# Kernel tuning notes

Measured on AMD Instinct MI355X. Metric: run time of the kernel, lower is better.

The kernel has to match this reference:

```python
import jax, jax.numpy as jnp
import numpy as np

B, F, N, NO = 1, 512, 8192, 21
L1, L2, L3 = 640, 256, 128


def setup_inputs() -> dict:
    key = jax.random.key(0)
    ks = jax.random.split(key, 32)
    rn = lambda k, s: jax.random.normal(k, s, dtype=jnp.float32)
    inp = {
        "emb1": rn(ks[0], (B, F, N)),
        "emb2": rn(ks[1], (B, F, N)),
        "t1": rn(ks[2], (B, 3, N)),
        "t2": rn(ks[3], (B, 3, N)),
        "obj": jax.random.randint(ks[4], (B, 1), 0, NO, dtype=jnp.int32),
    }
    # 1x1 Conv1d weights == dense (out,in) matrices + bias
    dims_r = [(L1, 2 * F), (L2, L1), (L3, L2), (NO * 4, L3)]
    dims_t = [(L1, 2 * F), (L2, L1), (L3, L2), (NO * 3, L3)]
    ki = 5
    for br, dims in (("r", dims_r), ("t", dims_t)):
        for i, (o, c) in enumerate(dims, start=1):
            inp[f"w{i}{br}"] = rn(ks[ki], (o, c)) * (1.0 / np.sqrt(c)); ki += 1
            inp[f"b{i}{br}"] = rn(ks[ki], (o,)) * 0.01; ki += 1
    return inp


def _knn1(ref, qry):
    # ref, qry: (3, N). For each query point j, index of nearest ref point.
    g = ref.T @ qry  # (N_ref, N_qry)
    d2 = jnp.sum(ref * ref, axis=0)[:, None] + jnp.sum(qry * qry, axis=0)[None, :] - 2.0 * g
    return jnp.argmin(d2, axis=0)  # (N_qry,)


def _branch(x, w1, b1, w2, b2, w3, b3, w4, b4):
    h = jax.nn.relu(w1 @ x + b1[:, None])
    h = jax.nn.relu(w2 @ h + b2[:, None])
    h = jax.nn.relu(w3 @ h + b3[:, None])
    return w4 @ h + b4[:, None]


def reference(emb1, emb2, t1, t2, obj,
              w1r, b1r, w2r, b2r, w3r, b3r, w4r, b4r,
              w1t, b1t, w2t, b2t, w3t, b3t, w4t, b4t):
    bs, num_feat, num_points = emb1.shape
    t1 = t1.reshape(bs, 3, -1)
    t2 = t2.reshape(bs, 3, -1)
    # brute-force 1-NN of each t2 point among t1 points (bs == 1)
    idx = _knn1(t1[0], t2[0])  # (N,) zero-based (torch code subtracts 1 from 1-based inds)
    emb1g = emb1[0][:, idx]  # gather matched features, (F, N)
    # torch.stack([emb1,emb2],dim=1).view(bs, 2F, N) == channel concat [emb1g; emb2]
    emb = jnp.concatenate([emb1g, emb2[0]], axis=0)  # (2F, N)
    rx = _branch(emb, w1r, b1r, w2r, b2r, w3r, b3r, w4r, b4r).reshape(NO, 4, num_points)
    tx = _branch(emb, w1t, b1t, w2t, b2t, w3t, b3t, w4t, b4t).reshape(NO, 3, num_points)
    obj0 = obj[0]  # (1,)
    out_rx = jnp.transpose(rx[obj0], (0, 2, 1))  # (1, N, 4)
    out_tx = jnp.transpose(tx[obj0], (0, 2, 1))  # (1, N, 3)
    return out_rx, out_tx
```

## Files before the change

kernel.cpp:

```cpp
#include <hip/hip_runtime.h>

typedef unsigned short u16;
typedef __bf16 bf16x8 __attribute__((ext_vector_type(8)));
typedef float f32x4 __attribute__((ext_vector_type(4)));

__device__ __forceinline__ float b2f(u16 v) {
    return __uint_as_float(((unsigned int)v) << 16);
}
__device__ __forceinline__ u16 f2b(float f) {
    unsigned int u = __float_as_uint(f);
    u += 0x7fffu + ((u >> 16) & 1u);
    return (u16)(u >> 16);
}

__device__ __forceinline__ void ld_lds16(const u16* g, u16* l) {
    __builtin_amdgcn_global_load_lds(
        (__attribute__((address_space(1))) void*)(uintptr_t)(const void*)g,
        (__attribute__((address_space(3))) void*)l, 16, 0, 0);
}

__global__ void pack_w_k(const float* __restrict__ w1r, const float* __restrict__ w1t,
                         const float* __restrict__ w2r, const float* __restrict__ w2t,
                         const float* __restrict__ w3r, const float* __restrict__ w3t,
                         u16* __restrict__ dst)
{
    size_t i = (size_t)blockIdx.x * 2048 + (size_t)threadIdx.x * 8;
    const float* src; size_t off;
    if (i < 655360)       { src = w1r; off = 0; }
    else if (i < 1310720) { src = w1t; off = 655360; }
    else if (i < 1474560) { src = w2r; off = 1310720; }
    else if (i < 1638400) { src = w2t; off = 1474560; }
    else if (i < 1671168) { src = w3r; off = 1638400; }
    else                  { src = w3t; off = 1671168; }
    const float4 lo = *(const float4*)(src + (i - off));
    const float4 hi = *(const float4*)(src + (i - off) + 4);
    ushort4 o0, o1;
    o0.x = f2b(lo.x); o0.y = f2b(lo.y); o0.z = f2b(lo.z); o0.w = f2b(lo.w);
    o1.x = f2b(hi.x); o1.y = f2b(hi.y); o1.z = f2b(hi.z); o1.w = f2b(hi.w);
    *(ushort4*)(dst + i) = o0;
    *(ushort4*)(dst + i + 4) = o1;
}

__global__ void knn_k(const float* __restrict__ t1, const float* __restrict__ t2,
                      unsigned long long* __restrict__ keys)
{
    __shared__ float4 ref[128];
    const int t = threadIdx.x;
    const int rs = blockIdx.x;
    const int qb = blockIdx.y;
    if (t < 128) {
        int i = rs * 128 + t;
        float x = t1[i], y = t1[8192 + i], z = t1[16384 + i];
        float rr = __fadd_rn(__fadd_rn(__fmul_rn(x, x), __fmul_rn(y, y)), __fmul_rn(z, z));
        ref[t] = make_float4(x, y, z, rr);
    }
    __syncthreads();

    float qx[8], qy[8], qz[8], qq[8], bestd[8];
    int besti[8];
    const int q0 = qb * 2048 + t;
#pragma unroll
    for (int j = 0; j < 8; ++j) {
        int q = q0 + j * 256;
        qx[j] = t2[q]; qy[j] = t2[8192 + q]; qz[j] = t2[16384 + q];
        qq[j] = __fadd_rn(__fadd_rn(__fmul_rn(qx[j], qx[j]), __fmul_rn(qy[j], qy[j])),
                          __fmul_rn(qz[j], qz[j]));
        bestd[j] = __uint_as_float(0x7f800000u);
        besti[j] = 0;
    }
    for (int i = 0; i < 128; ++i) {
        float4 r = ref[i];
        int ridx = rs * 128 + i;
#pragma unroll
        for (int j = 0; j < 8; ++j) {
            float g = __fmaf_rn(qz[j], r.z, __fmaf_rn(qy[j], r.y, __fmul_rn(qx[j], r.x)));
            float d2 = __fsub_rn(__fadd_rn(r.w, qq[j]), __fmul_rn(2.0f, g));
            if (d2 < bestd[j]) { bestd[j] = d2; besti[j] = ridx; }
        }
    }
#pragma unroll
    for (int j = 0; j < 8; ++j) {
        unsigned long long key =
            ((unsigned long long)__float_as_uint(bestd[j]) << 32) | (unsigned int)besti[j];
        atomicMin(&keys[q0 + j * 256], key);
    }
}

__global__ void transpose_k(const float* __restrict__ e1, const float* __restrict__ e2,
                            u16* __restrict__ o1, u16* __restrict__ o2)
{
    __shared__ float tile[64][65];
    const float* in = blockIdx.z ? e2 : e1;
    u16* out = blockIdx.z ? o2 : o1;
    const int ostride = blockIdx.z ? 1024 : 512;
    const int coff = blockIdx.z ? 512 : 0;
    const int t = threadIdx.x;
    const int n0 = blockIdx.x * 64, f0 = blockIdx.y * 64;
    const int c = t & 63, r4 = t >> 6;
#pragma unroll
    for (int p = 0; p < 16; ++p) {
        int fr = p * 4 + r4;
        tile[fr][c] = in[(size_t)(f0 + fr) * 8192 + n0 + c];
    }
    __syncthreads();
    const int fc = (t & 15) * 4;
    const int nr4 = t >> 4;
#pragma unroll
    for (int p = 0; p < 4; ++p) {
        int nr = p * 16 + nr4;
        ushort4 o;
        o.x = f2b(tile[fc + 0][nr]); o.y = f2b(tile[fc + 1][nr]);
        o.z = f2b(tile[fc + 2][nr]); o.w = f2b(tile[fc + 3][nr]);
        *(ushort4*)&out[(size_t)(n0 + nr) * ostride + coff + f0 + fc] = o;
    }
}

__global__ void gather_k(const unsigned long long* __restrict__ keys,
                         const u16* __restrict__ emb1t, u16* __restrict__ Xt)
{
    const int t = threadIdx.x, w = t >> 6, l = t & 63;
    const int nbase = blockIdx.x * 32;
#pragma unroll
    for (int it = 0; it < 8; ++it) {
        int n = nbase + it * 4 + w;
        int i = (int)(keys[n] & 0xffffffffu);
        const uint4* src = (const uint4*)(emb1t + (size_t)i * 512);
        uint4* dst = (uint4*)(Xt + (size_t)n * 1024);
        dst[l] = src[l];
    }
}

template <int TN>
__global__ __launch_bounds__(256) void gemm_bt(
    const u16* __restrict__ Ar, const u16* __restrict__ At,
    const float* __restrict__ biasr, const float* __restrict__ biast,
    const u16* __restrict__ Bt, u16* __restrict__ Ct,
    int Mh, int K, int bstride, int b_step, int ostride, int relu)
{
    constexpr int NJ = TN / 32;
    __shared__ __align__(16) u16 lds_a[128 * 32];
    __shared__ __align__(16) u16 lds_b[TN * 32];

    const int t = threadIdx.x;
    const int n0 = blockIdx.x * TN;
    const int m0 = blockIdx.y * 128;
    const int branch = blockIdx.z;

    const u16* A = branch ? At : Ar;
    const float* bias = branch ? biast : biasr;
    const int b_off = branch * b_step;
    const int out_off = branch * Mh;

    const int w = t >> 6, l = t & 63;
    const int sr = l >> 2, sc = (l & 3) * 8;

    const u16* gA0 = A + (size_t)(m0 + w * 32 + sr) * K + sc;
    const u16* gA1 = gA0 + (size_t)16 * K;
    u16* lA0 = &lds_a[w * 1024];
    u16* lA1 = lA0 + 512;

    const u16* gB0;
    const u16* gB1 = nullptr;
    u16 *lB0, *lB1 = nullptr;
    if (TN == 128) {
        gB0 = Bt + (size_t)(n0 + w * 32 + sr) * bstride + b_off + sc;
        gB1 = gB0 + (size_t)16 * bstride;
        lB0 = &lds_b[w * 1024];
        lB1 = lB0 + 512;
    } else {
        gB0 = Bt + (size_t)(n0 + w * 16 + sr) * bstride + b_off + sc;
        lB0 = &lds_b[w * 512];
    }

    const int wm = (w & 1) * 64;
    const int wn = (w >> 1) * (TN / 2);
    const int lrow = l & 15, quad = l >> 4;
    const u16* fa = &lds_a[(wm + lrow) * 32 + quad * 8];
    const u16* fb = &lds_b[(wn + lrow) * 32 + quad * 8];

    f32x4 acc[4][NJ];
#pragma unroll
    for (int i = 0; i < 4; ++i)
#pragma unroll
        for (int j = 0; j < NJ; ++j)
            acc[i][j] = (f32x4){0.f, 0.f, 0.f, 0.f};

    ld_lds16(gA0, lA0); ld_lds16(gA1, lA1);
    ld_lds16(gB0, lB0);
    if (TN == 128) ld_lds16(gB1, lB1);

    for (int kt = 0; kt < K; kt += 32) {
        __syncthreads();
        bf16x8 af[4], bfr[NJ];
#pragma unroll
        for (int i = 0; i < 4; ++i) af[i] = *(const bf16x8*)(fa + i * 16 * 32);
#pragma unroll
        for (int j = 0; j < NJ; ++j) bfr[j] = *(const bf16x8*)(fb + j * 16 * 32);
        __syncthreads();
        if (kt + 32 < K) {
            gA0 += 32; gA1 += 32; gB0 += 32;
            ld_lds16(gA0, lA0); ld_lds16(gA1, lA1);
            ld_lds16(gB0, lB0);
            if (TN == 128) { gB1 += 32; ld_lds16(gB1, lB1); }
        }
#pragma unroll
        for (int i = 0; i < 4; ++i)
#pragma unroll
            for (int j = 0; j < NJ; ++j)
                acc[i][j] = __builtin_amdgcn_mfma_f32_16x16x32_bf16(
                    af[i], bfr[j], acc[i][j], 0, 0, 0);
    }

#pragma unroll
    for (int i = 0; i < 4; ++i) {
        const int mbase = m0 + wm + i * 16 + quad * 4;
        const float4 bbv = *(const float4*)&bias[mbase];
#pragma unroll
        for (int j = 0; j < NJ; ++j) {
            const int n = n0 + wn + j * 16 + lrow;
            f32x4 v = acc[i][j];
            float x0 = v[0] + bbv.x, x1 = v[1] + bbv.y;
            float x2 = v[2] + bbv.z, x3 = v[3] + bbv.w;
            if (relu) {
                x0 = fmaxf(x0, 0.f); x1 = fmaxf(x1, 0.f);
                x2 = fmaxf(x2, 0.f); x3 = fmaxf(x3, 0.f);
            }
            ushort4 o;
            o.x = f2b(x0); o.y = f2b(x1); o.z = f2b(x2); o.w = f2b(x3);
            *(ushort4*)&Ct[(size_t)n * ostride + out_off + mbase] = o;
        }
    }
}

__global__ __launch_bounds__(256) void gemm3_final_k(
    const u16* __restrict__ Ar, const u16* __restrict__ At,
    const float* __restrict__ b3r, const float* __restrict__ b3t,
    const u16* __restrict__ Bt,
    const float* __restrict__ w4r, const float* __restrict__ b4r,
    const float* __restrict__ w4t, const float* __restrict__ b4t,
    const int* __restrict__ objp, float* __restrict__ out)
{
    __shared__ __align__(16) u16 lds_a[128 * 32];
    __shared__ __align__(16) u16 lds_b[64 * 32];
    __shared__ __align__(16) float lds_h[64 * 132];
    __shared__ __align__(16) float lds_w[4 * 132];

    const int t = threadIdx.x;
    const int n0 = blockIdx.x * 64;
    const int branch = blockIdx.y;

    const u16* A = branch ? At : Ar;
    const float* bias = branch ? b3t : b3r;
    const int b_off = branch * 256;

    const int w = t >> 6, l = t & 63;
    const int sr = l >> 2, sc = (l & 3) * 8;

    const u16* gA0 = A + (size_t)(w * 32 + sr) * 256 + sc;
    const u16* gA1 = gA0 + (size_t)16 * 256;
    u16* lA0 = &lds_a[w * 1024];
    u16* lA1 = lA0 + 512;

    const u16* gB0 = Bt + (size_t)(n0 + w * 16 + sr) * 512 + b_off + sc;
    u16* lB0 = &lds_b[w * 512];

    const int wm = (w & 1) * 64;
    const int wn = (w >> 1) * 32;
    const int lrow = l & 15, quad = l >> 4;
    const u16* fa = &lds_a[(wm + lrow) * 32 + quad * 8];
    const u16* fb = &lds_b[(wn + lrow) * 32 + quad * 8];

    f32x4 acc[4][2];
#pragma unroll
    for (int i = 0; i < 4; ++i)
#pragma unroll
        for (int j = 0; j < 2; ++j)
            acc[i][j] = (f32x4){0.f, 0.f, 0.f, 0.f};

    ld_lds16(gA0, lA0); ld_lds16(gA1, lA1);
    ld_lds16(gB0, lB0);

    for (int kt = 0; kt < 256; kt += 32) {
        __syncthreads();
        bf16x8 af[4], bfr[2];
#pragma unroll
        for (int i = 0; i < 4; ++i) af[i] = *(const bf16x8*)(fa + i * 16 * 32);
#pragma unroll
        for (int j = 0; j < 2; ++j) bfr[j] = *(const bf16x8*)(fb + j * 16 * 32);
        __syncthreads();
        if (kt + 32 < 256) {
            gA0 += 32; gA1 += 32; gB0 += 32;
            ld_lds16(gA0, lA0); ld_lds16(gA1, lA1);
            ld_lds16(gB0, lB0);
        }
#pragma unroll
        for (int i = 0; i < 4; ++i)
#pragma unroll
            for (int j = 0; j < 2; ++j)
                acc[i][j] = __builtin_amdgcn_mfma_f32_16x16x32_bf16(
                    af[i], bfr[j], acc[i][j], 0, 0, 0);
    }

#pragma unroll
    for (int i = 0; i < 4; ++i) {
        const int mbase = wm + i * 16 + quad * 4;
        const float4 bbv = *(const float4*)&bias[mbase];
#pragma unroll
        for (int j = 0; j < 2; ++j) {
            const int nl = wn + j * 16 + lrow;
            f32x4 v = acc[i][j];
            float4 x;
            x.x = fmaxf(v[0] + bbv.x, 0.f); x.y = fmaxf(v[1] + bbv.y, 0.f);
            x.z = fmaxf(v[2] + bbv.z, 0.f); x.w = fmaxf(v[3] + bbv.w, 0.f);
            *(float4*)&lds_h[nl * 132 + mbase] = x;
        }
    }
    const int o = objp[0];
    const int NR = branch ? 3 : 4;
    const float* w4 = branch ? w4t : w4r;
    if (t < 128) {
        for (int r = 0; r < NR; ++r)
            lds_w[r * 132 + t] = w4[(size_t)(o * NR + r) * 128 + t];
    }
    __syncthreads();

    const int nl = t >> 2, k = t & 3;
    if (k < NR) {
        const float4* hp = (const float4*)&lds_h[nl * 132];
        const float4* wp4 = (const float4*)&lds_w[k * 132];
        float s = 0.f;
#pragma unroll
        for (int m4 = 0; m4 < 32; ++m4) {
            float4 h = hp[m4], ww = wp4[m4];
            s = fmaf(h.x, ww.x, s); s = fmaf(h.y, ww.y, s);
            s = fmaf(h.z, ww.z, s); s = fmaf(h.w, ww.w, s);
        }
        const int n = n0 + nl;
        if (branch == 0) out[(size_t)n * 4 + k] = s + b4r[o * 4 + k];
        else             out[32768 + (size_t)n * 3 + k] = s + b4t[o * 3 + k];
    }
}

extern "C" void kernel_launch(void* const* d_in, const int* in_sizes, int n_in,
                              void* d_out, int out_size, void* d_ws, size_t ws_size,
                              hipStream_t stream)
{
    const float* emb1 = (const float*)d_in[0];
    const float* emb2 = (const float*)d_in[1];
    const float* t1   = (const float*)d_in[2];
    const float* t2   = (const float*)d_in[3];
    const int*   obj  = (const int*)d_in[4];
    const float* w1r = (const float*)d_in[5];  const float* b1r = (const float*)d_in[6];
    const float* w2r = (const float*)d_in[7];  const float* b2r = (const float*)d_in[8];
    const float* w3r = (const float*)d_in[9];  const float* b3r = (const float*)d_in[10];
    const float* w4r = (const float*)d_in[11]; const float* b4r = (const float*)d_in[12];
    const float* w1t = (const float*)d_in[13]; const float* b1t = (const float*)d_in[14];
    const float* w2t = (const float*)d_in[15]; const float* b2t = (const float*)d_in[16];
    const float* w3t = (const float*)d_in[17]; const float* b3t = (const float*)d_in[18];
    const float* w4t = (const float*)d_in[19]; const float* b4t = (const float*)d_in[20];

    char* ws = (char*)d_ws;
    unsigned long long* keys = (unsigned long long*)ws;
    u16* emb1t = (u16*)(ws + (1u << 16));
    u16* Xt    = (u16*)(ws + (1u << 16) + (8u << 20));
    u16* h1t   = (u16*)(ws + (1u << 16) + (24u << 20));
    u16* wp    = (u16*)(ws + (1u << 16) + (44u << 20));
    u16* h2t   = emb1t;

    u16* w1rp = wp;            u16* w1tp = wp + 655360;
    u16* w2rp = wp + 1310720;  u16* w2tp = wp + 1474560;
    u16* w3rp = wp + 1638400;  u16* w3tp = wp + 1671168;

    hipMemsetAsync(keys, 0xFF, 8192 * sizeof(unsigned long long), stream);
    pack_w_k<<<832, 256, 0, stream>>>(w1r, w1t, w2r, w2t, w3r, w3t, wp);
    knn_k<<<dim3(64, 4), 256, 0, stream>>>(t1, t2, keys);
    transpose_k<<<dim3(128, 8, 2), 256, 0, stream>>>(emb1, emb2, emb1t, Xt);
    gather_k<<<256, 256, 0, stream>>>(keys, emb1t, Xt);
    gemm_bt<128><<<dim3(64, 5, 2), 256, 0, stream>>>(w1rp, w1tp, b1r, b1t, Xt,  h1t, 640, 1024, 1024,   0, 1280, 1);
    gemm_bt<64><<<dim3(128, 2, 2), 256, 0, stream>>>(w2rp, w2tp, b2r, b2t, h1t, h2t, 256,  640, 1280, 640,  512, 1);
    gemm3_final_k<<<dim3(128, 2), 256, 0, stream>>>(w3rp, w3tp, b3r, b3t, h2t,
                                                    w4r, b4r, w4t, b4t, obj, (float*)d_out);
}
```

Baseline: 198.8 us.

## Fuse kNN gather into first GEMM's B-operand loads, drop gather kernel

Removes the separate gather kernel and the concatenated Xt buffer. The first-layer GEMM now reads B rows directly from the transposed emb1 at the kNN index for the first 512 K columns, and from transposed emb2 for the rest. The r and t weight halves are treated as a single M=1280 problem rather than a branch grid dimension. This saves a kernel launch and an 8192x1024 bf16 write plus re-read, but the emb1 part of the B operand now comes from scattered rows. The second GEMM is de-templated to its 64-wide form.

```diff
diff --git a/kernel.cpp b/kernel.cpp
--- a/kernel.cpp
+++ b/kernel.cpp
@@ -92,8 +92,6 @@
     __shared__ float tile[64][65];
     const float* in = blockIdx.z ? e2 : e1;
     u16* out = blockIdx.z ? o2 : o1;
-    const int ostride = blockIdx.z ? 1024 : 512;
-    const int coff = blockIdx.z ? 512 : 0;
     const int t = threadIdx.x;
     const int n0 = blockIdx.x * 64, f0 = blockIdx.y * 64;
     const int c = t & 63, r4 = t >> 6;
@@ -111,38 +109,111 @@
         ushort4 o;
         o.x = f2b(tile[fc + 0][nr]); o.y = f2b(tile[fc + 1][nr]);
         o.z = f2b(tile[fc + 2][nr]); o.w = f2b(tile[fc + 3][nr]);
-        *(ushort4*)&out[(size_t)(n0 + nr) * ostride + coff + f0 + fc] = o;
-    }
-}
-
-__global__ void gather_k(const unsigned long long* __restrict__ keys,
-                         const u16* __restrict__ emb1t, u16* __restrict__ Xt)
-{
-    const int t = threadIdx.x, w = t >> 6, l = t & 63;
-    const int nbase = blockIdx.x * 32;
-#pragma unroll
-    for (int it = 0; it < 8; ++it) {
-        int n = nbase + it * 4 + w;
-        int i = (int)(keys[n] & 0xffffffffu);
-        const uint4* src = (const uint4*)(emb1t + (size_t)i * 512);
-        uint4* dst = (uint4*)(Xt + (size_t)n * 1024);
-        dst[l] = src[l];
-    }
-}
-
-template <int TN>
+        *(ushort4*)&out[(size_t)(n0 + nr) * 512 + f0 + fc] = o;
+    }
+}
+
+__global__ __launch_bounds__(256) void gemm1_k(
+    const u16* __restrict__ A,
+    const float* __restrict__ b1r, const float* __restrict__ b1t,
+    const unsigned long long* __restrict__ keys,
+    const u16* __restrict__ e1t, const u16* __restrict__ e2t,
+    u16* __restrict__ Ct)
+{
+    __shared__ __align__(16) u16 lds_a[128 * 32];
+    __shared__ __align__(16) u16 lds_b[128 * 32];
+
+    const int t = threadIdx.x;
+    const int n0 = blockIdx.x * 128;
+    const int m0 = blockIdx.y * 128;
+    const int w = t >> 6, l = t & 63;
+    const int sr = l >> 2, sc = (l & 3) * 8;
+
+    const u16* gA0 = A + (size_t)(m0 + w * 32 + sr) * 1024 + sc;
+    const u16* gA1 = gA0 + (size_t)16 * 1024;
+    u16* lA0 = &lds_a[w * 1024];
+    u16* lA1 = lA0 + 512;
+
+    const int r0 = n0 + w * 32 + sr, r1 = r0 + 16;
+    const int i0 = (int)(keys[r0] & 0xffffffffu);
+    const int i1 = (int)(keys[r1] & 0xffffffffu);
+    const u16* pI0 = e1t + (size_t)i0 * 512 + sc;
+    const u16* pI1 = e1t + (size_t)i1 * 512 + sc;
+    const u16* pD0 = e2t + (size_t)r0 * 512 + sc;
+    const u16* pD1 = e2t + (size_t)r1 * 512 + sc;
+    u16* lB0 = &lds_b[w * 1024];
+    u16* lB1 = lB0 + 512;
+
+    const int wm = (w & 1) * 64;
+    const int wn = (w >> 1) * 64;
+    const int lrow = l & 15, quad = l >> 4;
+    const u16* fa = &lds_a[(wm + lrow) * 32 + quad * 8];
+    const u16* fb = &lds_b[(wn + lrow) * 32 + quad * 8];
+
+    f32x4 acc[4][4];
+#pragma unroll
+    for (int i = 0; i < 4; ++i)
+#pragma unroll
+        for (int j = 0; j < 4; ++j)
+            acc[i][j] = (f32x4){0.f, 0.f, 0.f, 0.f};
+
+    ld_lds16(gA0, lA0); ld_lds16(gA1, lA1);
+    ld_lds16(pI0, lB0); ld_lds16(pI1, lB1);
+
+    for (int kt = 0; kt < 1024; kt += 32) {
+        __syncthreads();
+        bf16x8 af[4], bfr[4];
+#pragma unroll
+        for (int i = 0; i < 4; ++i) af[i] = *(const bf16x8*)(fa + i * 16 * 32);
+#pragma unroll
+        for (int j = 0; j < 4; ++j) bfr[j] = *(const bf16x8*)(fb + j * 16 * 32);
+        __syncthreads();
+        const int kn = kt + 32;
+        if (kn < 1024) {
+            gA0 += 32; gA1 += 32;
+            const u16* s0 = (kn < 512) ? pI0 + kn : pD0 + (kn - 512);
+            const u16* s1 = (kn < 512) ? pI1 + kn : pD1 + (kn - 512);
+            ld_lds16(gA0, lA0); ld_lds16(gA1, lA1);
+            ld_lds16(s0, lB0); ld_lds16(s1, lB1);
+        }
+#pragma unroll
+        for (int i = 0; i < 4; ++i)
+#pragma unroll
+            for (int j = 0; j < 4; ++j)
+                acc[i][j] = __builtin_amdgcn_mfma_f32_16x16x32_bf16(
+                    af[i], bfr[j], acc[i][j], 0, 0, 0);
+    }
+
+    const float* bias = (m0 < 640) ? b1r : b1t;
+    const int boff = (m0 < 640) ? 0 : 640;
+#pragma unroll
+    for (int i = 0; i < 4; ++i) {
+        const int mbase = m0 + wm + i * 16 + quad * 4;
+        const float4 bbv = *(const float4*)&bias[mbase - boff];
+#pragma unroll
+        for (int j = 0; j < 4; ++j) {
+            const int n = n0 + wn + j * 16 + lrow;
+            f32x4 v = acc[i][j];
+            float x0 = fmaxf(v[0] + bbv.x, 0.f), x1 = fmaxf(v[1] + bbv.y, 0.f);
+            float x2 = fmaxf(v[2] + bbv.z, 0.f), x3 = fmaxf(v[3] + bbv.w, 0.f);
+            ushort4 o;
+            o.x = f2b(x0); o.y = f2b(x1); o.z = f2b(x2); o.w = f2b(x3);
+            *(ushort4*)&Ct[(size_t)n * 1280 + mbase] = o;
+        }
+    }
+}
+
 __global__ __launch_bounds__(256) void gemm_bt(
     const u16* __restrict__ Ar, const u16* __restrict__ At,
     const float* __restrict__ biasr, const float* __restrict__ biast,
     const u16* __restrict__ Bt, u16* __restrict__ Ct,
-    int Mh, int K, int bstride, int b_step, int ostride, int relu)
-{
-    constexpr int NJ = TN / 32;
+    int Mh, int K, int bstride, int b_step, int ostride)
+{
     __shared__ __align__(16) u16 lds_a[128 * 32];
-    __shared__ __align__(16) u16 lds_b[TN * 32];
+    __shared__ __align__(16) u16 lds_b[64 * 32];
 
     const int t = threadIdx.x;
-    const int n0 = blockIdx.x * TN;
+    const int n0 = blockIdx.x * 64;
     const int m0 = blockIdx.y * 128;
     const int branch = blockIdx.z;
 
@@ -159,54 +230,42 @@
     u16* lA0 = &lds_a[w * 1024];
     u16* lA1 = lA0 + 512;
 
-    const u16* gB0;
-    const u16* gB1 = nullptr;
-    u16 *lB0, *lB1 = nullptr;
-    if (TN == 128) {
-        gB0 = Bt + (size_t)(n0 + w * 32 + sr) * bstride + b_off + sc;
-        gB1 = gB0 + (size_t)16 * bstride;
-        lB0 = &lds_b[w * 1024];
-        lB1 = lB0 + 512;
-    } else {
-        gB0 = Bt + (size_t)(n0 + w * 16 + sr) * bstride + b_off + sc;
-        lB0 = &lds_b[w * 512];
-    }
+    const u16* gB0 = Bt + (size_t)(n0 + w * 16 + sr) * bstride + b_off + sc;
+    u16* lB0 = &lds_b[w * 512];
 
     const int wm = (w & 1) * 64;
-    const int wn = (w >> 1) * (TN / 2);
+    const int wn = (w >> 1) * 32;
     const int lrow = l & 15, quad = l >> 4;
     const u16* fa = &lds_a[(wm + lrow) * 32 + quad * 8];
     const u16* fb = &lds_b[(wn + lrow) * 32 + quad * 8];
 
-    f32x4 acc[4][NJ];
+    f32x4 acc[4][2];
 #pragma unroll
     for (int i = 0; i < 4; ++i)
 #pragma unroll
-        for (int j = 0; j < NJ; ++j)
+        for (int j = 0; j < 2; ++j)
             acc[i][j] = (f32x4){0.f, 0.f, 0.f, 0.f};
 
     ld_lds16(gA0, lA0); ld_lds16(gA1, lA1);
     ld_lds16(gB0, lB0);
-    if (TN == 128) ld_lds16(gB1, lB1);
 
     for (int kt = 0; kt < K; kt += 32) {
         __syncthreads();
-        bf16x8 af[4], bfr[NJ];
+        bf16x8 af[4], bfr[2];
 #pragma unroll
         for (int i = 0; i < 4; ++i) af[i] = *(const bf16x8*)(fa + i * 16 * 32);
 #pragma unroll
-        for (int j = 0; j < NJ; ++j) bfr[j] = *(const bf16x8*)(fb + j * 16 * 32);
+        for (int j = 0; j < 2; ++j) bfr[j] = *(const bf16x8*)(fb + j * 16 * 32);
         __syncthreads();
         if (kt + 32 < K) {
             gA0 += 32; gA1 += 32; gB0 += 32;
             ld_lds16(gA0, lA0); ld_lds16(gA1, lA1);
             ld_lds16(gB0, lB0);
-            if (TN == 128) { gB1 += 32; ld_lds16(gB1, lB1); }
         }
 #pragma unroll
         for (int i = 0; i < 4; ++i)
 #pragma unroll
-            for (int j = 0; j < NJ; ++j)
+            for (int j = 0; j < 2; ++j)
                 acc[i][j] = __builtin_amdgcn_mfma_f32_16x16x32_bf16(
                     af[i], bfr[j], acc[i][j], 0, 0, 0);
     }
@@ -216,15 +275,11 @@
         const int mbase = m0 + wm + i * 16 + quad * 4;
         const float4 bbv = *(const float4*)&bias[mbase];
 #pragma unroll
-        for (int j = 0; j < NJ; ++j) {
+        for (int j = 0; j < 2; ++j) {
             const int n = n0 + wn + j * 16 + lrow;
             f32x4 v = acc[i][j];
-            float x0 = v[0] + bbv.x, x1 = v[1] + bbv.y;
-            float x2 = v[2] + bbv.z, x3 = v[3] + bbv.w;
-            if (relu) {
-                x0 = fmaxf(x0, 0.f); x1 = fmaxf(x1, 0.f);
-                x2 = fmaxf(x2, 0.f); x3 = fmaxf(x3, 0.f);
-            }
+            float x0 = fmaxf(v[0] + bbv.x, 0.f), x1 = fmaxf(v[1] + bbv.y, 0.f);
+            float x2 = fmaxf(v[2] + bbv.z, 0.f), x3 = fmaxf(v[3] + bbv.w, 0.f);
             ushort4 o;
             o.x = f2b(x0); o.y = f2b(x1); o.z = f2b(x2); o.w = f2b(x3);
             *(ushort4*)&Ct[(size_t)n * ostride + out_off + mbase] = o;
@@ -361,11 +416,11 @@
 
     char* ws = (char*)d_ws;
     unsigned long long* keys = (unsigned long long*)ws;
-    u16* emb1t = (u16*)(ws + (1u << 16));
-    u16* Xt    = (u16*)(ws + (1u << 16) + (8u << 20));
-    u16* h1t   = (u16*)(ws + (1u << 16) + (24u << 20));
-    u16* wp    = (u16*)(ws + (1u << 16) + (44u << 20));
-    u16* h2t   = emb1t;
+    u16* e1t = (u16*)(ws + (1u << 16));
+    u16* e2t = (u16*)(ws + (1u << 16) + (8u << 20));
+    u16* h1t = (u16*)(ws + (1u << 16) + (16u << 20));
+    u16* wp  = (u16*)(ws + (1u << 16) + (36u << 20));
+    u16* h2t = e1t;
 
     u16* w1rp = wp;            u16* w1tp = wp + 655360;
     u16* w2rp = wp + 1310720;  u16* w2tp = wp + 1474560;
@@ -374,10 +429,9 @@
     hipMemsetAsync(keys, 0xFF, 8192 * sizeof(unsigned long long), stream);
     pack_w_k<<<832, 256, 0, stream>>>(w1r, w1t, w2r, w2t, w3r, w3t, wp);
     knn_k<<<dim3(64, 4), 256, 0, stream>>>(t1, t2, keys);
-    transpose_k<<<dim3(128, 8, 2), 256, 0, stream>>>(emb1, emb2, emb1t, Xt);
-    gather_k<<<256, 256, 0, stream>>>(keys, emb1t, Xt);
-    gemm_bt<128><<<dim3(64, 5, 2), 256, 0, stream>>>(w1rp, w1tp, b1r, b1t, Xt,  h1t, 640, 1024, 1024,   0, 1280, 1);
-    gemm_bt<64><<<dim3(128, 2, 2), 256, 0, stream>>>(w2rp, w2tp, b2r, b2t, h1t, h2t, 256,  640, 1280, 640,  512, 1);
+    transpose_k<<<dim3(128, 8, 2), 256, 0, stream>>>(emb1, emb2, e1t, e2t);
+    gemm1_k<<<dim3(64, 10), 256, 0, stream>>>(w1rp, b1r, b1t, keys, e1t, e2t, h1t);
+    gemm_bt<<<dim3(128, 2, 2), 256, 0, stream>>>(w2rp, w2tp, b2r, b2t, h1t, h2t, 256, 640, 1280, 640, 512);
     gemm3_final_k<<<dim3(128, 2), 256, 0, stream>>>(w3rp, w3tp, b3r, b3t, h2t,
                                                     w4r, b4r, w4t, b4t, obj, (float*)d_out);
 }
```

Measured after the change: 201.7 us. No clear change (+1.4%).
